# Performance work log

Hardware: AMD Instinct MI355X
Metric: run time of the kernel (lower is better)

## Reference

```python
import jax, jax.numpy as jnp
import numpy as np

WIDTH = 256
BASE = 4
BUTTERFLY_COUNT = 4  # 256 == 4**4


def butterfly_permutation(width, group_size, multiplier):
    """Fixed channel permutation from ButterflyPermutation (kernel_size=1)."""
    batch_size = group_size * multiplier
    idx = np.arange(width)
    idx_in_group = idx % group_size
    group_idx = (idx % batch_size) // group_size
    batch_idx = (idx % width) // batch_size
    return group_idx + multiplier * idx_in_group + batch_size * batch_idx


# permutation after butterfly conv i (i = 0,1,2): group_size = base**(i+1), multiplier = base
PERMS = [butterfly_permutation(WIDTH, BASE ** (i + 1), BASE) for i in range(BUTTERFLY_COUNT - 1)]


def gconv1x1(x, w):
    """Grouped 1x1 conv. x: [B, G*I, H, W]; w: [G, O, I] -> [B, G*O, H, W]."""
    B, C, H, Wd = x.shape
    G, O, I = w.shape
    xg = x.reshape(B, G, I, H, Wd)
    y = jnp.einsum('goi,bgihw->bgohw', w, xg)
    return y.reshape(B, G * O, H, Wd)


def setup_inputs() -> dict:
    key = jax.random.key(0)
    ks = jax.random.split(key, 5)
    B, C, H, W = 32, WIDTH, 56, 56
    G, O, I = 64, 4, 4
    scale = 1.0 / np.sqrt(I)
    x = jax.random.normal(ks[0], (B, C, H, W), dtype=jnp.float32)
    ws = [jax.random.normal(ks[i + 1], (G, O, I), dtype=jnp.float32) * scale for i in range(4)]
    return {"x": x, "w0": ws[0], "w1": ws[1], "w2": ws[2], "w3": ws[3]}


def reference(x, w0, w1, w2, w3):
    # butterfly chain: conv -> perm -> conv -> perm -> conv -> perm -> conv
    weights = [w0, w1, w2, w3]
    for i in range(BUTTERFLY_COUNT):
        x = gconv1x1(x, weights[i])
        if i != BUTTERFLY_COUNT - 1:
            x = x[:, PERMS[i], :, :]
    return x
```

## Files before the change

### kernel.cpp

```cpp
#include <hip/hip_runtime.h>


#define HW 3136
#define TILE_PX 256
#define NT 13

typedef float f32x4 __attribute__((ext_vector_type(4)));

__device__ __forceinline__ void fma4(f32x4& acc, float s, const f32x4& a) {
    acc = s * a + acc;
}

__global__ __launch_bounds__(256, 2)
void butterfly_fused_v2(const float* __restrict__ x,
                        const float* __restrict__ w0,
                        const float* __restrict__ w1,
                        const float* __restrict__ w2,
                        const float* __restrict__ w3,
                        float* __restrict__ out) {
    __shared__ float buf[64 * TILE_PX];

    const int l  = threadIdx.x & 63;
    const int wv = __builtin_amdgcn_readfirstlane((int)(threadIdx.x >> 6));
    const int bid  = blockIdx.x;
    const int tile = bid % NT;
    const int rem  = bid / NT;
    const int e    = rem & 3;
    const int img  = rem >> 2;

    const int pix  = tile * TILE_PX + 4 * l;
    const bool ok  = pix < HW;
    const int pixc = ok ? pix : 0;
    const int ibase = img * 256 * HW + pixc;
    const int obase = img * 256 * HW + pix;

    f32x4 xr[16];
#pragma unroll
    for (int i = 0; i < 4; ++i)
#pragma unroll
        for (int j = 0; j < 4; ++j) {
            const int c = (e << 6) | (wv << 4) | (i << 2) | j;
            xr[4 * i + j] = *reinterpret_cast<const f32x4*>(x + ibase + c * HW);
        }

    f32x4 b0[16];
#pragma unroll
    for (int i = 0; i < 4; ++i) {
        const float* wg = w0 + (((e << 4) | (wv << 2) | i) << 4);
#pragma unroll
        for (int o = 0; o < 4; ++o) {
            f32x4 acc = wg[o * 4 + 0] * xr[4 * i + 0];
            fma4(acc, wg[o * 4 + 1], xr[4 * i + 1]);
            fma4(acc, wg[o * 4 + 2], xr[4 * i + 2]);
            fma4(acc, wg[o * 4 + 3], xr[4 * i + 3]);
            b0[4 * i + o] = acc;
        }
    }

#pragma unroll
    for (int d1 = 0; d1 < 4; ++d1) {
        const float* wg = w1 + (((e << 4) | (wv << 2) | d1) << 4);
#pragma unroll
        for (int o = 0; o < 4; ++o) {
            f32x4 acc = wg[o * 4 + 0] * b0[0 + d1];
            fma4(acc, wg[o * 4 + 1], b0[4 + d1]);
            fma4(acc, wg[o * 4 + 2], b0[8 + d1]);
            fma4(acc, wg[o * 4 + 3], b0[12 + d1]);
            const int lc = (wv << 4) | (d1 << 2) | o;
            *reinterpret_cast<f32x4*>(buf + lc * TILE_PX + 4 * l) = acc;
        }
    }

    __syncthreads();

    const int f = wv;
    f32x4 yr[16];
#pragma unroll
    for (int i = 0; i < 4; ++i)
#pragma unroll
        for (int i2 = 0; i2 < 4; ++i2) {
            const int lc = (i << 4) | (i2 << 2) | f;
            yr[4 * i + i2] = *reinterpret_cast<const f32x4*>(buf + lc * TILE_PX + 4 * l);
        }

    f32x4 b2[16];
#pragma unroll
    for (int i = 0; i < 4; ++i) {
        const float* wg = w2 + (((e << 4) | (f << 2) | i) << 4);
#pragma unroll
        for (int o = 0; o < 4; ++o) {
            f32x4 acc = wg[o * 4 + 0] * yr[4 * i + 0];
            fma4(acc, wg[o * 4 + 1], yr[4 * i + 1]);
            fma4(acc, wg[o * 4 + 2], yr[4 * i + 2]);
            fma4(acc, wg[o * 4 + 3], yr[4 * i + 3]);
            b2[4 * i + o] = acc;
        }
    }

#pragma unroll
    for (int g2 = 0; g2 < 4; ++g2) {
        const float* wg = w3 + (((g2 << 4) | (e << 2) | f) << 4);
#pragma unroll
        for (int o = 0; o < 4; ++o) {
            f32x4 acc = wg[o * 4 + 0] * b2[0 + g2];
            fma4(acc, wg[o * 4 + 1], b2[4 + g2]);
            fma4(acc, wg[o * 4 + 2], b2[8 + g2]);
            fma4(acc, wg[o * 4 + 3], b2[12 + g2]);
            if (ok) {
                const int c = (g2 << 6) | (e << 4) | (f << 2) | o;
                __builtin_nontemporal_store(acc,
                    reinterpret_cast<f32x4*>(out + obase + c * HW));
            }
        }
    }
}

extern "C" void kernel_launch(void* const* d_in, const int* in_sizes, int n_in,
                              void* d_out, int out_size, void* d_ws, size_t ws_size,
                              hipStream_t stream) {
    const float* x  = (const float*)d_in[0];
    const float* w0 = (const float*)d_in[1];
    const float* w1 = (const float*)d_in[2];
    const float* w2 = (const float*)d_in[3];
    const float* w3 = (const float*)d_in[4];
    float* out = (float*)d_out;

    dim3 grid(32 * 4 * NT);
    dim3 block(256);
    butterfly_fused_v2<<<grid, block, 0, stream>>>(x, w0, w1, w2, w3, out);
}
```

Baseline: 38.80 us.

## Keep all 64 channels per thread in registers, removing LDS exchange and barrier

Each thread now owns 2 pixels across all 64 channels of its group-of-64, so the stage-2 channel shuffle between waves happens in registers instead of going through shared memory with a __syncthreads. Tiles grow to 512 pixels with float2 loads and stores, and out-of-range threads exit early. This removes LDS traffic and the barrier. In exchange it needs about 128 registers for the input plus temporaries, which may cut occupancy or cause spills, and it uses narrower 8-byte memory accesses.

After: 44.91 us. 15.8% more time.

```diff
diff --git a/kernel.cpp b/kernel.cpp
--- a/kernel.cpp
+++ b/kernel.cpp
@@ -2,114 +2,95 @@
 
 
 #define HW 3136
-#define TILE_PX 256
-#define NT 13
+#define TILE_PX 512
+#define NT 7
 
-typedef float f32x4 __attribute__((ext_vector_type(4)));
-
-__device__ __forceinline__ void fma4(f32x4& acc, float s, const f32x4& a) {
-    acc = s * a + acc;
-}
+typedef float f32x2 __attribute__((ext_vector_type(2)));
 
 __global__ __launch_bounds__(256, 2)
-void butterfly_fused_v2(const float* __restrict__ x,
-                        const float* __restrict__ w0,
-                        const float* __restrict__ w1,
-                        const float* __restrict__ w2,
-                        const float* __restrict__ w3,
-                        float* __restrict__ out) {
-    __shared__ float buf[64 * TILE_PX];
-
-    const int l  = threadIdx.x & 63;
-    const int wv = __builtin_amdgcn_readfirstlane((int)(threadIdx.x >> 6));
+void butterfly_v3(const float* __restrict__ x,
+                  const float* __restrict__ w0,
+                  const float* __restrict__ w1,
+                  const float* __restrict__ w2,
+                  const float* __restrict__ w3,
+                  float* __restrict__ out) {
     const int bid  = blockIdx.x;
     const int tile = bid % NT;
     const int rem  = bid / NT;
     const int e    = rem & 3;
     const int img  = rem >> 2;
 
-    const int pix  = tile * TILE_PX + 4 * l;
-    const bool ok  = pix < HW;
-    const int pixc = ok ? pix : 0;
-    const int ibase = img * 256 * HW + pixc;
-    const int obase = img * 256 * HW + pix;
+    const int p = tile * TILE_PX + 2 * (int)threadIdx.x;
+    if (p >= HW) return;
 
-    f32x4 xr[16];
+    const int ibase = img * 256 * HW + (e << 6) * HW + p;
+    const int obase = img * 256 * HW + p;
+
+    f32x2 r[64];
 #pragma unroll
-    for (int i = 0; i < 4; ++i)
+    for (int k = 0; k < 64; ++k)
+        r[k] = *reinterpret_cast<const f32x2*>(x + ibase + k * HW);
+
 #pragma unroll
-        for (int j = 0; j < 4; ++j) {
-            const int c = (e << 6) | (wv << 4) | (i << 2) | j;
-            xr[4 * i + j] = *reinterpret_cast<const f32x4*>(x + ibase + c * HW);
-        }
-
-    f32x4 b0[16];
+    for (int v = 0; v < 4; ++v) {
 #pragma unroll
-    for (int i = 0; i < 4; ++i) {
-        const float* wg = w0 + (((e << 4) | (wv << 2) | i) << 4);
+        for (int i = 0; i < 4; ++i) {
+            const float* wg = w0 + (((e << 4) | (v << 2) | i) << 4);
+            const f32x2 in0 = r[v * 16 + i * 4 + 0];
+            const f32x2 in1 = r[v * 16 + i * 4 + 1];
+            const f32x2 in2 = r[v * 16 + i * 4 + 2];
+            const f32x2 in3 = r[v * 16 + i * 4 + 3];
 #pragma unroll
-        for (int o = 0; o < 4; ++o) {
-            f32x4 acc = wg[o * 4 + 0] * xr[4 * i + 0];
-            fma4(acc, wg[o * 4 + 1], xr[4 * i + 1]);
-            fma4(acc, wg[o * 4 + 2], xr[4 * i + 2]);
-            fma4(acc, wg[o * 4 + 3], xr[4 * i + 3]);
-            b0[4 * i + o] = acc;
+            for (int o = 0; o < 4; ++o)
+                r[v * 16 + i * 4 + o] =
+                    wg[o * 4 + 0] * in0 + wg[o * 4 + 1] * in1 +
+                    wg[o * 4 + 2] * in2 + wg[o * 4 + 3] * in3;
         }
     }
 
 #pragma unroll
-    for (int d1 = 0; d1 < 4; ++d1) {
-        const float* wg = w1 + (((e << 4) | (wv << 2) | d1) << 4);
+    for (int v = 0; v < 4; ++v) {
+        f32x2 t16[16];
 #pragma unroll
-        for (int o = 0; o < 4; ++o) {
-            f32x4 acc = wg[o * 4 + 0] * b0[0 + d1];
-            fma4(acc, wg[o * 4 + 1], b0[4 + d1]);
-            fma4(acc, wg[o * 4 + 2], b0[8 + d1]);
-            fma4(acc, wg[o * 4 + 3], b0[12 + d1]);
-            const int lc = (wv << 4) | (d1 << 2) | o;
-            *reinterpret_cast<f32x4*>(buf + lc * TILE_PX + 4 * l) = acc;
+        for (int d1 = 0; d1 < 4; ++d1) {
+            const float* wg = w1 + (((e << 4) | (v << 2) | d1) << 4);
+#pragma unroll
+            for (int o = 0; o < 4; ++o)
+                t16[d1 * 4 + o] =
+                    wg[o * 4 + 0] * r[v * 16 + 0 * 4 + d1] +
+                    wg[o * 4 + 1] * r[v * 16 + 1 * 4 + d1] +
+                    wg[o * 4 + 2] * r[v * 16 + 2 * 4 + d1] +
+                    wg[o * 4 + 3] * r[v * 16 + 3 * 4 + d1];
         }
-    }
-
-    __syncthreads();
-
-    const int f = wv;
-    f32x4 yr[16];
 #pragma unroll
-    for (int i = 0; i < 4; ++i)
-#pragma unroll
-        for (int i2 = 0; i2 < 4; ++i2) {
-            const int lc = (i << 4) | (i2 << 2) | f;
-            yr[4 * i + i2] = *reinterpret_cast<const f32x4*>(buf + lc * TILE_PX + 4 * l);
-        }
-
-    f32x4 b2[16];
-#pragma unroll
-    for (int i = 0; i < 4; ++i) {
-        const float* wg = w2 + (((e << 4) | (f << 2) | i) << 4);
-#pragma unroll
-        for (int o = 0; o < 4; ++o) {
-            f32x4 acc = wg[o * 4 + 0] * yr[4 * i + 0];
-            fma4(acc, wg[o * 4 + 1], yr[4 * i + 1]);
-            fma4(acc, wg[o * 4 + 2], yr[4 * i + 2]);
-            fma4(acc, wg[o * 4 + 3], yr[4 * i + 3]);
-            b2[4 * i + o] = acc;
-        }
+        for (int k = 0; k < 16; ++k) r[v * 16 + k] = t16[k];
     }
 
 #pragma unroll
-    for (int g2 = 0; g2 < 4; ++g2) {
-        const float* wg = w3 + (((g2 << 4) | (e << 2) | f) << 4);
+    for (int f = 0; f < 4; ++f) {
+        f32x2 b2[16];
 #pragma unroll
-        for (int o = 0; o < 4; ++o) {
-            f32x4 acc = wg[o * 4 + 0] * b2[0 + g2];
-            fma4(acc, wg[o * 4 + 1], b2[4 + g2]);
-            fma4(acc, wg[o * 4 + 2], b2[8 + g2]);
-            fma4(acc, wg[o * 4 + 3], b2[12 + g2]);
-            if (ok) {
+        for (int i = 0; i < 4; ++i) {
+            const float* wg = w2 + (((e << 4) | (f << 2) | i) << 4);
+#pragma unroll
+            for (int o = 0; o < 4; ++o)
+                b2[i * 4 + o] =
+                    wg[o * 4 + 0] * r[i * 16 + 0 * 4 + f] +
+                    wg[o * 4 + 1] * r[i * 16 + 1 * 4 + f] +
+                    wg[o * 4 + 2] * r[i * 16 + 2 * 4 + f] +
+                    wg[o * 4 + 3] * r[i * 16 + 3 * 4 + f];
+        }
+#pragma unroll
+        for (int g2 = 0; g2 < 4; ++g2) {
+            const float* wg = w3 + (((g2 << 4) | (e << 2) | f) << 4);
+#pragma unroll
+            for (int o = 0; o < 4; ++o) {
+                const f32x2 acc =
+                    wg[o * 4 + 0] * b2[0 + g2] + wg[o * 4 + 1] * b2[4 + g2] +
+                    wg[o * 4 + 2] * b2[8 + g2] + wg[o * 4 + 3] * b2[12 + g2];
                 const int c = (g2 << 6) | (e << 4) | (f << 2) | o;
                 __builtin_nontemporal_store(acc,
-                    reinterpret_cast<f32x4*>(out + obase + c * HW));
+                    reinterpret_cast<f32x2*>(out + obase + c * HW));
             }
         }
     }
@@ -127,5 +108,5 @@
 
     dim3 grid(32 * 4 * NT);
     dim3 block(256);
-    butterfly_fused_v2<<<grid, block, 0, stream>>>(x, w0, w1, w2, w3, out);
+    butterfly_v3<<<grid, block, 0, stream>>>(x, w0, w1, w2, w3, out);
 }
```
